# Kernel tuning notes

Hardware: AMD Instinct MI355X
Metric: run time of the kernel (lower is better)

## Reference

```python
import jax, jax.numpy as jnp
import numpy as np

B, N, M, H, NH = 8, 1024, 512, 1024, 4
DH = H // NH          # 256 main attention head size
CDH = (H // 4) // 4   # 64  cross attention qk head size
EPS = 1e-12


def _ln(x, g, b):
    mu = jnp.mean(x, axis=-1, keepdims=True)
    var = jnp.mean((x - mu) ** 2, axis=-1, keepdims=True)
    return (x - mu) / jnp.sqrt(var + EPS) * g + b


def _heads(x, nh):
    b, n, d = x.shape
    return x.reshape(b, n, nh, d // nh).transpose(0, 2, 1, 3)  # [b,nh,n,dh]


def setup_inputs() -> dict:
    key = jax.random.key(0)
    ks = iter(jax.random.split(key, 64))
    nk = lambda: next(ks)
    w = lambda *s: jax.random.normal(nk(), s, jnp.float32) * 0.02
    inp = {}
    inp["hidden_states"] = jax.random.normal(nk(), (B, N, H), jnp.float32)
    inp["attention_mask"] = jnp.ones((B, N), jnp.float32)
    inp["structure_mask"] = (jax.random.uniform(nk(), (B, 3, N, N)) < 0.2).astype(jnp.float32)
    inp["Sentence_em"] = w(1, B, N, H)
    inp["entity_id_em"] = w(1, B, N, H)
    inp["cross_struct_mask"] = (jax.random.uniform(nk(), (B, 1, N, M)) < 0.3).astype(jnp.float32)
    inp["encoder_hidden_states"] = jax.random.normal(nk(), (1, B, M, H), jnp.float32)
    inp["encoder_attention_mask"] = jnp.ones((B, M), jnp.float32)
    # ---- Struct_SelfAttention params ----
    inp["Wq"] = w(H, 3 * DH); inp["bq"] = jnp.zeros(3 * DH)
    inp["Wk"] = w(H, 3 * DH); inp["bk"] = jnp.zeros(3 * DH)
    inp["Wv"] = w(H, H);      inp["bv"] = jnp.zeros(H)
    inp["Wq1"] = w(H, DH);    inp["bq1"] = jnp.zeros(DH)
    inp["Wk1"] = w(H, DH);    inp["bk1"] = jnp.zeros(DH)
    inp["ln_g"] = jnp.ones(H); inp["ln_b"] = jnp.zeros(H)
    inp["gnn_W"] = w(H, H); inp["gnn_b"] = jnp.zeros(H)
    inp["gnn_ln_g"] = jnp.ones(H); inp["gnn_ln_b"] = jnp.zeros(H)
    # ---- Cross_Attention params ----
    inp["cWq"] = w(H, H // 4); inp["cbq"] = jnp.zeros(H // 4)
    inp["cWk"] = w(H, H // 4); inp["cbk"] = jnp.zeros(H // 4)
    inp["cWv"] = w(H, H);      inp["cbv"] = jnp.zeros(H)
    inp["cWo"] = w(H, H);      inp["cbo"] = jnp.zeros(H)
    inp["cWg"] = w(2 * H, H);  inp["cbg"] = jnp.full((H,), -1.0, jnp.float32)  # Gate bias init -1
    inp["c_ln_g"] = jnp.ones(H); inp["c_ln_b"] = jnp.zeros(H)
    # ---- Output block params ----
    inp["oW1"] = w(H, H); inp["ob1"] = jnp.zeros(H)
    inp["o_ln1_g"] = jnp.ones(H); inp["o_ln1_b"] = jnp.zeros(H)
    inp["oW2"] = w(H, 2 * H); inp["ob2"] = jnp.zeros(2 * H)
    inp["oW3"] = w(2 * H, H); inp["ob3"] = jnp.zeros(H)
    inp["o_ln3_g"] = jnp.ones(H); inp["o_ln3_b"] = jnp.zeros(H)
    inp["layer_idx"] = 0
    return inp


def reference(hidden_states, attention_mask, structure_mask, Sentence_em, entity_id_em,
              cross_struct_mask, encoder_hidden_states, encoder_attention_mask,
              Wq, bq, Wk, bk, Wv, bv, Wq1, bq1, Wk1, bk1, ln_g, ln_b,
              gnn_W, gnn_b, gnn_ln_g, gnn_ln_b,
              cWq, cbq, cWk, cbk, cWv, cbv, cWo, cbo, cWg, cbg, c_ln_g, c_ln_b,
              oW1, ob1, o_ln1_g, o_ln1_b, oW2, ob2, oW3, ob3, o_ln3_g, o_ln3_b,
              layer_idx):
    hs = hidden_states
    q = _heads(hs @ Wq + bq, 3)          # [B,3,N,DH]
    k = _heads(hs @ Wk + bk, 3)
    v = _heads(hs @ Wv + bv, 4)          # [B,4,N,DH]
    s1 = jnp.einsum('bhnd,bhmd->bhnm', q, k)          # unscaled scores, 3 heads
    am0 = (1.0 - attention_mask)[:, None, None, :] * -10000.0
    s3 = s1 + am0
    # valid off-diagonal pairs mask (broadcasts over the 3 heads)
    pair = attention_mask[:, None, :, None] * attention_mask[:, None, None, :]
    idxw = ((pair * (1.0 - jnp.eye(N, dtype=jnp.float32))) > 0.5).astype(jnp.float32)  # [B,1,N,N]
    # sigmoid focal loss (gamma=2, alpha=0.25, mean over selected elements)
    p = jax.nn.sigmoid(s3)
    t = structure_mask
    fl = 0.25 * t * (1.0 - p) ** 2 * (-jax.nn.log_sigmoid(s3)) \
       + 0.75 * (1.0 - t) * p ** 2 * (-jax.nn.log_sigmoid(-s3))
    loss = jnp.sum(fl * idxw) / (3.0 * jnp.sum(idxw))
    # structural attention path (3 heads)
    s1 = s1 / np.float32(np.sqrt(DH)) + (1.0 - structure_mask) * -10000.0
    probs1 = jax.nn.softmax(s1, axis=-1)
    # positional/structural single-head path
    h1 = _ln(hs + Sentence_em[layer_idx] + entity_id_em[layer_idx], ln_g, ln_b)
    q1 = _heads(h1 @ Wq1 + bq1, 1)
    k1 = _heads(h1 @ Wk1 + bk1, 1)
    s2 = jnp.einsum('bhnd,bhmd->bhnm', q1, k1) / np.float32(np.sqrt(DH)) + am0
    probs2 = jax.nn.softmax(s2, axis=-1)
    probs = jnp.concatenate([probs2, probs1], axis=1)  # [B,4,N,N]
    ctx = jnp.einsum('bhnm,bhmd->bhnd', probs, v).transpose(0, 2, 1, 3).reshape(B, N, H)
    gnn_out = _ln(ctx @ gnn_W + gnn_b, gnn_ln_g, gnn_ln_b)
    # ---- Cross attention ----
    enc = encoder_hidden_states[layer_idx]            # [B,M,H]
    cq = _heads(gnn_out @ cWq + cbq, 4)               # [B,4,N,CDH]
    ck = _heads(enc @ cWk + cbk, 4)                   # [B,4,M,CDH]
    cv = _heads(enc @ cWv + cbv, 4)                   # [B,4,M,DH]
    cs = jnp.einsum('bhnd,bhmd->bhnm', cq, ck) / np.float32(np.sqrt(CDH))
    cs = cs + (1.0 - cross_struct_mask) * -10000.0
    cp = jax.nn.softmax(cs, axis=-1)
    cctx = jnp.einsum('bhnm,bhmd->bhnd', cp, cv).transpose(0, 2, 1, 3).reshape(B, N, H)
    cctx = cctx @ cWo + cbo
    gate = jax.nn.sigmoid(jnp.concatenate([gnn_out, cctx], axis=-1) @ cWg + cbg)
    cross_out = _ln(gate * cctx + (1.0 - gate) * gnn_out, c_ln_g, c_ln_b)
    # ---- Output block (gated FFN) ----
    h = _ln(cross_out @ oW1 + ob1 + hidden_states, o_ln1_g, o_ln1_b)
    h3 = jax.nn.gelu(h @ oW2 + ob2, approximate=False) @ oW3 + ob3
    out = _ln(h3 + h, o_ln3_g, o_ln3_b)
    return out, loss
```

## Files before the change

### kernel.cpp

```cpp
#include <hip/hip_runtime.h>
#include <math.h>

#define DEV __device__ __forceinline__

typedef short short8 __attribute__((ext_vector_type(8)));
typedef float float4v __attribute__((ext_vector_type(4)));

DEV unsigned short f2bf(float f) {
    union { float f; unsigned u; } v; v.f = f;
    unsigned r = v.u + 0x7FFFu + ((v.u >> 16) & 1u);
    return (unsigned short)(r >> 16);
}

DEV float block_reduce(float v, int mode) {
    #pragma unroll
    for (int off = 32; off; off >>= 1) {
        float o = __shfl_xor(v, off);
        v = mode ? fmaxf(v, o) : (v + o);
    }
    __shared__ float sbuf[4];
    __syncthreads();
    if ((threadIdx.x & 63) == 0) sbuf[threadIdx.x >> 6] = v;
    __syncthreads();
    float r = sbuf[0];
    #pragma unroll
    for (int w = 1; w < 4; w++) r = mode ? fmaxf(r, sbuf[w]) : (r + sbuf[w]);
    return r;
}

template <bool BIAS, bool ACCUM, bool GELU>
__global__ __launch_bounds__(256) void gemm_bf16_kernel(
    const unsigned short* __restrict__ A, int lda,
    const unsigned short* __restrict__ Bt, int ldb,
    const float* __restrict__ bias,
    float* __restrict__ Cf, unsigned short* __restrict__ Cb,
    int N, int K)
{
    __shared__ unsigned short As[128 * 40];
    __shared__ unsigned short Bs[128 * 40];
    const int tid = threadIdx.x;
    const int w = tid >> 6, lane = tid & 63;
    const int l15 = lane & 15, quad = lane >> 4;
    const int m0 = blockIdx.y * 128, n0 = blockIdx.x * 128;
    const int wm = (w >> 1) * 64, wn = (w & 1) * 64;

    float4v acc[4][4];
    #pragma unroll
    for (int i = 0; i < 4; i++)
        #pragma unroll
        for (int j = 0; j < 4; j++) acc[i][j] = (float4v){0.f, 0.f, 0.f, 0.f};

    for (int k0 = 0; k0 < K; k0 += 32) {
        __syncthreads();
        #pragma unroll
        for (int i = 0; i < 2; i++) {
            const int c = tid + i * 256;
            const int row = c >> 2, kc = (c & 3) * 8;
            *(uint4*)(As + row * 40 + kc) =
                *(const uint4*)(A + (size_t)(m0 + row) * lda + k0 + kc);
            *(uint4*)(Bs + row * 40 + kc) =
                *(const uint4*)(Bt + (size_t)(n0 + row) * ldb + k0 + kc);
        }
        __syncthreads();
        short8 Af[4], Bf[4];
        #pragma unroll
        for (int mt = 0; mt < 4; mt++)
            Af[mt] = *(const short8*)(As + (wm + mt * 16 + l15) * 40 + quad * 8);
        #pragma unroll
        for (int nt = 0; nt < 4; nt++)
            Bf[nt] = *(const short8*)(Bs + (wn + nt * 16 + l15) * 40 + quad * 8);
        #pragma unroll
        for (int mt = 0; mt < 4; mt++)
            #pragma unroll
            for (int nt = 0; nt < 4; nt++)
                acc[mt][nt] = __builtin_amdgcn_mfma_f32_16x16x32_bf16(
                    Af[mt], Bf[nt], acc[mt][nt], 0, 0, 0);
    }

    #pragma unroll
    for (int nt = 0; nt < 4; nt++) {
        const int n = n0 + wn + nt * 16 + l15;
        const float bv = BIAS ? bias[n] : 0.f;
        #pragma unroll
        for (int mt = 0; mt < 4; mt++) {
            #pragma unroll
            for (int r = 0; r < 4; r++) {
                const int m = m0 + wm + mt * 16 + quad * 4 + r;
                const size_t off = (size_t)m * N + n;
                float v = acc[mt][nt][r] + bv;
                if (ACCUM) v += Cf[off];
                if (GELU) v = 0.5f * v * (1.f + erff(v * 0.70710678118654752f));
                if (Cf) Cf[off] = v;
                if (Cb) Cb[off] = f2bf(v);
            }
        }
    }
}

__global__ __launch_bounds__(256) void wtrans_kernel(
    const float* __restrict__ W, unsigned short* __restrict__ Wt, int K, int N)
{
    __shared__ float t[32][33];
    const int n0 = blockIdx.x * 32, k0 = blockIdx.y * 32;
    const int c = threadIdx.x & 31, r8 = threadIdx.x >> 5;
    #pragma unroll
    for (int i = 0; i < 4; i++) {
        const int r = r8 + i * 8;
        t[r][c] = W[(size_t)(k0 + r) * N + n0 + c];
    }
    __syncthreads();
    #pragma unroll
    for (int i = 0; i < 4; i++) {
        const int r = r8 + i * 8;
        Wt[(size_t)(n0 + r) * K + k0 + c] = f2bf(t[c][r]);
    }
}

__global__ __launch_bounds__(256) void trans_kernel(
    const unsigned short* __restrict__ v, unsigned short* __restrict__ Vt,
    int R, int C)
{
    __shared__ unsigned short t[32][33];
    const int b = blockIdx.z, r0 = blockIdx.x * 32, c0 = blockIdx.y * 32;
    const int c = threadIdx.x & 31, r8 = threadIdx.x >> 5;
    #pragma unroll
    for (int i = 0; i < 4; i++) {
        const int r = r8 + i * 8;
        t[r][c] = v[((size_t)b * R + r0 + r) * C + c0 + c];
    }
    __syncthreads();
    #pragma unroll
    for (int i = 0; i < 4; i++) {
        const int r = r8 + i * 8;
        Vt[((size_t)b * C + c0 + r) * R + r0 + c] = t[c][r];
    }
}

__global__ __launch_bounds__(256) void castbf_kernel(
    const float* __restrict__ x, unsigned short* __restrict__ y)
{
    const size_t i = ((size_t)blockIdx.x * 256 + threadIdx.x) * 4;
    float4 v = *(const float4*)(x + i);
    ushort4 o;
    o.x = f2bf(v.x); o.y = f2bf(v.y); o.z = f2bf(v.z); o.w = f2bf(v.w);
    *(ushort4*)(y + i) = o;
}

DEV void ln_finish(float4 xv, const float* __restrict__ g,
                   const float* __restrict__ bb, float* __restrict__ outf,
                   unsigned short* __restrict__ outb, size_t base)
{
    float s  = xv.x + xv.y + xv.z + xv.w;
    float s2 = xv.x * xv.x + xv.y * xv.y + xv.z * xv.z + xv.w * xv.w;
    #pragma unroll
    for (int off = 32; off; off >>= 1) {
        s += __shfl_xor(s, off);
        s2 += __shfl_xor(s2, off);
    }
    __shared__ float sa[4], sb[4];
    if ((threadIdx.x & 63) == 0) {
        sa[threadIdx.x >> 6] = s; sb[threadIdx.x >> 6] = s2;
    }
    __syncthreads();
    s  = sa[0] + sa[1] + sa[2] + sa[3];
    s2 = sb[0] + sb[1] + sb[2] + sb[3];
    const float mu  = s * (1.f / 1024.f);
    const float var = fmaxf(s2 * (1.f / 1024.f) - mu * mu, 0.f);
    const float inv = rsqrtf(var + 1e-12f);
    const int tid = threadIdx.x;
    float4 gv = ((const float4*)g)[tid];
    float4 bv = ((const float4*)bb)[tid];
    float4 o;
    o.x = (xv.x - mu) * inv * gv.x + bv.x;
    o.y = (xv.y - mu) * inv * gv.y + bv.y;
    o.z = (xv.z - mu) * inv * gv.z + bv.z;
    o.w = (xv.w - mu) * inv * gv.w + bv.w;
    if (outf) ((float4*)(outf + base))[tid] = o;
    if (outb) {
        ushort4 ob;
        ob.x = f2bf(o.x); ob.y = f2bf(o.y); ob.z = f2bf(o.z); ob.w = f2bf(o.w);
        ((ushort4*)(outb + base))[tid] = ob;
    }
}

__global__ __launch_bounds__(256) void ln_kernel(
    const float* __restrict__ x, const float* __restrict__ r1,
    const float* __restrict__ r2, const float* __restrict__ g,
    const float* __restrict__ bb, float* __restrict__ outf,
    unsigned short* __restrict__ outb)
{
    const size_t base = (size_t)blockIdx.x * 1024;
    const int tid = threadIdx.x;
    float4 xv = ((const float4*)(x + base))[tid];
    if (r1) {
        float4 a = ((const float4*)(r1 + base))[tid];
        xv.x += a.x; xv.y += a.y; xv.z += a.z; xv.w += a.w;
    }
    if (r2) {
        float4 a = ((const float4*)(r2 + base))[tid];
        xv.x += a.x; xv.y += a.y; xv.z += a.z; xv.w += a.w;
    }
    ln_finish(xv, g, bb, outf, outb, base);
}

__global__ __launch_bounds__(256) void gate_ln_kernel(
    const float* __restrict__ gpre, const float* __restrict__ co,
    const float* __restrict__ gn, const float* __restrict__ g,
    const float* __restrict__ bb, float* __restrict__ outf,
    unsigned short* __restrict__ outb)
{
    const size_t base = (size_t)blockIdx.x * 1024;
    const int tid = threadIdx.x;
    float4 gp = ((const float4*)(gpre + base))[tid];
    float4 cv = ((const float4*)(co + base))[tid];
    float4 gv = ((const float4*)(gn + base))[tid];
    float4 xv; float s;
    s = 1.f / (1.f + __expf(-gp.x)); xv.x = s * cv.x + (1.f - s) * gv.x;
    s = 1.f / (1.f + __expf(-gp.y)); xv.y = s * cv.y + (1.f - s) * gv.y;
    s = 1.f / (1.f + __expf(-gp.z)); xv.z = s * cv.z + (1.f - s) * gv.z;
    s = 1.f / (1.f + __expf(-gp.w)); xv.w = s * cv.w + (1.f - s) * gv.w;
    ln_finish(xv, g, bb, outf, outb, base);
}

__global__ __launch_bounds__(256) void attn_mfma_kernel(
    const unsigned short* __restrict__ qh,
    const unsigned short* __restrict__ kh,
    const unsigned short* __restrict__ q1,
    const unsigned short* __restrict__ k1,
    const unsigned short* __restrict__ Vt,
    const float* __restrict__ am,
    const float* __restrict__ smask,
    unsigned short* __restrict__ ctx,
    float* __restrict__ nump, float* __restrict__ denp)
{
    const int nb = blockIdx.x;
    const int h  = blockIdx.y;
    const int b  = blockIdx.z;
    const int tid = threadIdx.x;
    const int w = tid >> 6, lane = tid & 63;
    const int l15 = lane & 15, quad = lane >> 4;
    const int n0 = nb * 64;

    __shared__ unsigned short Ks[32 * 264];
    __shared__ unsigned short Vs[256 * 40];
    __shared__ unsigned short Ps[4][16 * 40];

    const unsigned short* qsrc; const unsigned short* ksrc; int kpitch, koff;
    if (h == 0) { qsrc = q1; ksrc = k1; kpitch = 256; koff = 0; }
    else        { qsrc = qh; ksrc = kh; kpitch = 768; koff = (h - 1) * 256; }

    short8 Qf[8];
    {
        const unsigned short* qrow =
            qsrc + (size_t)(b * 1024 + n0 + w * 16 + l15) * kpitch + koff;
        #pragma unroll
        for (int kk = 0; kk < 8; kk++)
            Qf[kk] = *(const short8*)(qrow + kk * 32 + quad * 8);
    }

    float4v O[16];
    #pragma unroll
    for (int i = 0; i < 16; i++) O[i] = (float4v){0.f, 0.f, 0.f, 0.f};
    float lsum[4] = {0.f, 0.f, 0.f, 0.f};
    float flsum = 0.f, dencnt = 0.f;
    const int nrow_base = n0 + w * 16 + quad * 4;
    float amn[4];
    #pragma unroll
    for (int r = 0; r < 4; r++) amn[r] = am[b * 1024 + nrow_base + r];
    const float* smbase = (h > 0)
        ? smask + ((size_t)b * 3 + (h - 1)) * 1024 * 1024 : nullptr;

    for (int m0 = 0; m0 < 1024; m0 += 32) {
        __syncthreads();
        for (int c = tid; c < 1024; c += 256) {
            const int row = c >> 5, kc = (c & 31) * 8;
            *(uint4*)(Ks + row * 264 + kc) =
                *(const uint4*)(ksrc + (size_t)(b * 1024 + m0 + row) * kpitch + koff + kc);
        }
        for (int c = tid; c < 1024; c += 256) {
            const int d = c >> 2, mc = (c & 3) * 8;
            *(uint4*)(Vs + d * 40 + mc) =
                *(const uint4*)(Vt + (size_t)(b * 1024 + h * 256 + d) * 1024 + m0 + mc);
        }
        __syncthreads();

        float4v S[2];
        #pragma unroll
        for (int st = 0; st < 2; st++) {
            float4v a = (float4v){0.f, 0.f, 0.f, 0.f};
            #pragma unroll
            for (int kk = 0; kk < 8; kk++) {
                short8 Kf = *(const short8*)(Ks + (st * 16 + l15) * 264 + kk * 32 + quad * 8);
                a = __builtin_amdgcn_mfma_f32_16x16x32_bf16(Qf[kk], Kf, a, 0, 0, 0);
            }
            S[st] = a;
        }

        float e[2][4];
        #pragma unroll
        for (int st = 0; st < 2; st++) {
            const int mcol = m0 + st * 16 + l15;
            const float amm = am[b * 1024 + mcol];
            const float am0 = (1.f - amm) * (-10000.f);
            #pragma unroll
            for (int r = 0; r < 4; r++) {
                const float sraw = S[st][r];
                float scv;
                if (h > 0) {
                    const int nrow = nrow_base + r;
                    const float t  = smbase[(size_t)nrow * 1024 + mcol];
                    const float s3 = sraw + am0;
                    const float idxw =
                        ((amn[r] * amm * ((mcol == nrow) ? 0.f : 1.f)) > 0.5f) ? 1.f : 0.f;
                    const float E = __expf(-fabsf(s3));
                    const float L = __logf(1.f + E);
                    const float R = 1.f / (1.f + E);
                    const float p = (s3 >= 0.f) ? R : E * R;
                    const float sp = fmaxf(s3, 0.f) + L;
                    const float omp = 1.f - p;
                    flsum += idxw * (0.25f * t * omp * omp * (sp - s3)
                                   + 0.75f * (1.f - t) * p * p * sp);
                    dencnt += idxw;
                    scv = sraw * 0.0625f + (1.f - t) * (-10000.f);
                } else {
                    scv = sraw * 0.0625f + am0;
                }
                const float ev = __expf(fminf(scv, 30.f));
                e[st][r] = ev;
                lsum[r] += ev;
            }
        }

        #pragma unroll
        for (int st = 0; st < 2; st++)
            #pragma unroll
            for (int r = 0; r < 4; r++)
                Ps[w][(quad * 4 + r) * 40 + st * 16 + l15] = f2bf(e[st][r]);
        const short8 Pf = *(const short8*)(&Ps[w][l15 * 40 + quad * 8]);
        #pragma unroll
        for (int dt = 0; dt < 16; dt++) {
            short8 Vf = *(const short8*)(Vs + (dt * 16 + l15) * 40 + quad * 8);
            O[dt] = __builtin_amdgcn_mfma_f32_16x16x32_bf16(Pf, Vf, O[dt], 0, 0, 0);
        }
    }

    float rinv[4];
    #pragma unroll
    for (int r = 0; r < 4; r++) {
        float s = lsum[r];
        #pragma unroll
        for (int off = 8; off; off >>= 1) s += __shfl_xor(s, off);
        rinv[r] = 1.f / s;
    }
    #pragma unroll
    for (int dt = 0; dt < 16; dt++)
        #pragma unroll
        for (int r = 0; r < 4; r++)
            ctx[(size_t)(b * 1024 + nrow_base + r) * 1024 + h * 256 + dt * 16 + l15]
                = f2bf(O[dt][r] * rinv[r]);

    if (h > 0) {
        const float fb = block_reduce(flsum, 0);
        if (tid == 0) nump[(b * 3 + (h - 1)) * 16 + nb] = fb;
        if (h == 1) {
            const float db = block_reduce(dencnt, 0);
            if (tid == 0) denp[b * 16 + nb] = db;
        }
    }
}

__global__ __launch_bounds__(256) void cross_mfma_kernel(
    const unsigned short* __restrict__ cq,
    const unsigned short* __restrict__ ck,
    const unsigned short* __restrict__ cvt,
    const float* __restrict__ csm,
    unsigned short* __restrict__ cctx)
{
    const int nb = blockIdx.x;
    const int h  = blockIdx.y;
    const int b  = blockIdx.z;
    const int tid = threadIdx.x;
    const int w = tid >> 6, lane = tid & 63;
    const int l15 = lane & 15, quad = lane >> 4;
    const int n0 = nb * 64;

    __shared__ unsigned short Ks[32 * 72];
    __shared__ unsigned short Vs[256 * 40];
    __shared__ unsigned short Ps[4][16 * 40];

    short8 Qf[2];
    {
        const unsigned short* qrow =
            cq + (size_t)(b * 1024 + n0 + w * 16 + l15) * 256 + h * 64;
        #pragma unroll
        for (int kk = 0; kk < 2; kk++)
            Qf[kk] = *(const short8*)(qrow + kk * 32 + quad * 8);
    }

    float4v O[16];
    #pragma unroll
    for (int i = 0; i < 16; i++) O[i] = (float4v){0.f, 0.f, 0.f, 0.f};
    float lsum[4] = {0.f, 0.f, 0.f, 0.f};
    const int nrow_base = n0 + w * 16 + quad * 4;

    for (int m0 = 0; m0 < 512; m0 += 32) {
        __syncthreads();
        if (tid < 256) {
            const int row = tid >> 3, kc = (tid & 7) * 8;
            *(uint4*)(Ks + row * 72 + kc) =
                *(const uint4*)(ck + (size_t)(b * 512 + m0 + row) * 256 + h * 64 + kc);
        }
        for (int c = tid; c < 1024; c += 256) {
            const int d = c >> 2, mc = (c & 3) * 8;
            *(uint4*)(Vs + d * 40 + mc) =
                *(const uint4*)(cvt + (size_t)(b * 1024 + h * 256 + d) * 512 + m0 + mc);
        }
        __syncthreads();

        float e[2][4];
        #pragma unroll
        for (int st = 0; st < 2; st++) {
            float4v a = (float4v){0.f, 0.f, 0.f, 0.f};
            #pragma unroll
            for (int kk = 0; kk < 2; kk++) {
                short8 Kf = *(const short8*)(Ks + (st * 16 + l15) * 72 + kk * 32 + quad * 8);
                a = __builtin_amdgcn_mfma_f32_16x16x32_bf16(Qf[kk], Kf, a, 0, 0, 0);
            }
            const int mcol = m0 + st * 16 + l15;
            #pragma unroll
            for (int r = 0; r < 4; r++) {
                const float msk = csm[(size_t)(b * 1024 + nrow_base + r) * 512 + mcol];
                const float scv = a[r] * 0.125f + (1.f - msk) * (-10000.f);
                const float ev = __expf(fminf(scv, 30.f));
                e[st][r] = ev;
                lsum[r] += ev;
            }
        }

        #pragma unroll
        for (int st = 0; st < 2; st++)
            #pragma unroll
            for (int r = 0; r < 4; r++)
                Ps[w][(quad * 4 + r) * 40 + st * 16 + l15] = f2bf(e[st][r]);
        const short8 Pf = *(const short8*)(&Ps[w][l15 * 40 + quad * 8]);
        #pragma unroll
        for (int dt = 0; dt < 16; dt++) {
            short8 Vf = *(const short8*)(Vs + (dt * 16 + l15) * 40 + quad * 8);
            O[dt] = __builtin_amdgcn_mfma_f32_16x16x32_bf16(Pf, Vf, O[dt], 0, 0, 0);
        }
    }

    float rinv[4];
    #pragma unroll
    for (int r = 0; r < 4; r++) {
        float s = lsum[r];
        #pragma unroll
        for (int off = 8; off; off >>= 1) s += __shfl_xor(s, off);
        rinv[r] = 1.f / s;
    }
    #pragma unroll
    for (int dt = 0; dt < 16; dt++)
        #pragma unroll
        for (int r = 0; r < 4; r++)
            cctx[(size_t)(b * 1024 + nrow_base + r) * 1024 + h * 256 + dt * 16 + l15]
                = f2bf(O[dt][r] * rinv[r]);
}

__global__ __launch_bounds__(256) void loss_reduce_kernel(
    const float* __restrict__ nump, const float* __restrict__ denp,
    float* __restrict__ out)
{
    __shared__ double sn[256], sd[256];
    const int tid = threadIdx.x;
    double ns = 0.0, ds = 0.0;
    for (int i = tid; i < 384; i += 256) ns += (double)nump[i];
    for (int i = tid; i < 128; i += 256) ds += (double)denp[i];
    sn[tid] = ns; sd[tid] = ds;
    __syncthreads();
    for (int off = 128; off; off >>= 1) {
        if (tid < off) { sn[tid] += sn[tid + off]; sd[tid] += sd[tid + off]; }
        __syncthreads();
    }
    if (tid == 0) out[0] = (float)(sn[0] / (3.0 * sd[0]));
}

extern "C" void kernel_launch(void* const* d_in, const int* in_sizes, int n_in,
                              void* d_out, int out_size, void* d_ws, size_t ws_size,
                              hipStream_t stream)
{
    (void)in_sizes; (void)n_in; (void)out_size; (void)ws_size;
    const float* hs   = (const float*)d_in[0];
    const float* am   = (const float*)d_in[1];
    const float* smask= (const float*)d_in[2];
    const float* sent = (const float*)d_in[3];
    const float* ent  = (const float*)d_in[4];
    const float* csm  = (const float*)d_in[5];
    const float* enc  = (const float*)d_in[6];
    const float* Wq  = (const float*)d_in[8];  const float* bq  = (const float*)d_in[9];
    const float* Wk  = (const float*)d_in[10]; const float* bk  = (const float*)d_in[11];
    const float* Wv  = (const float*)d_in[12]; const float* bv  = (const float*)d_in[13];
    const float* Wq1 = (const float*)d_in[14]; const float* bq1 = (const float*)d_in[15];
    const float* Wk1 = (const float*)d_in[16]; const float* bk1 = (const float*)d_in[17];
    const float* ln_g= (const float*)d_in[18]; const float* ln_b= (const float*)d_in[19];
    const float* gW  = (const float*)d_in[20]; const float* gb  = (const float*)d_in[21];
    const float* gng = (const float*)d_in[22]; const float* gnb = (const float*)d_in[23];
    const float* cWq = (const float*)d_in[24]; const float* cbq = (const float*)d_in[25];
    const float* cWk = (const float*)d_in[26]; const float* cbk = (const float*)d_in[27];
    const float* cWv = (const float*)d_in[28]; const float* cbv = (const float*)d_in[29];
    const float* cWo = (const float*)d_in[30]; const float* cbo = (const float*)d_in[31];
    const float* cWg = (const float*)d_in[32]; const float* cbg = (const float*)d_in[33];
    const float* clg = (const float*)d_in[34]; const float* clb = (const float*)d_in[35];
    const float* oW1 = (const float*)d_in[36]; const float* ob1 = (const float*)d_in[37];
    const float* l1g = (const float*)d_in[38]; const float* l1b = (const float*)d_in[39];
    const float* oW2 = (const float*)d_in[40]; const float* ob2 = (const float*)d_in[41];
    const float* oW3 = (const float*)d_in[42]; const float* ob3 = (const float*)d_in[43];
    const float* l3g = (const float*)d_in[44]; const float* l3b = (const float*)d_in[45];
    float* out = (float*)d_out;

    typedef unsigned short ush;
    char* wsb = (char*)d_ws;
    ush* WT   = (ush*)wsb;
    ush* wqT  = WT;             ush* wkT  = WT + 786432;   ush* wvT  = WT + 1572864;
    ush* wq1T = WT + 2621440;   ush* wk1T = WT + 2883584;  ush* gWT_ = WT + 3145728;
    ush* cWqT = WT + 4194304;   ush* cWkT = WT + 4456448;  ush* cWvT = WT + 4718592;
    ush* cWoT = WT + 5767168;   ush* cWgT = WT + 6815744;  ush* oW1T = WT + 8912896;
    ush* oW2T = WT + 9961472;   ush* oW3T = WT + 12058624;
    ush*  hs_bf   = (ush*)(wsb + 28311552);
    ush*  enc_bf  = (ush*)(wsb + 45088768);
    ush*  q_bf    = (ush*)(wsb + 53477376);
    ush*  k_bf    = (ush*)(wsb + 66060288);
    ush*  v_bf    = (ush*)(wsb + 78643200);
    ush*  Vt      = (ush*)(wsb + 95420416);
    ush*  h1_bf   = (ush*)(wsb + 112197632);
    ush*  q1_bf   = (ush*)(wsb + 128974848);
    ush*  k1_bf   = (ush*)(wsb + 133169152);
    ush*  ctx_bf  = (ush*)(wsb + 137363456);
    float* nump   = (float*)(wsb + 154140672);
    float* denp   = (float*)(wsb + 154142208);
    float* gnn_f  = (float*)(wsb + 154144768);
    float* gnnout_f = (float*)(wsb + 187699200);
    ush*  gnnout_b  = (ush*)(wsb + 221253632);
    ush*  cq_b      = (ush*)(wsb + 53477376);
    ush*  ck_b      = (ush*)(wsb + 66060288);
    ush*  cv_b      = (ush*)(wsb + 78643200);
    ush*  cctx_b    = (ush*)(wsb + 95420416);
    ush*  cvt       = (ush*)(wsb + 238030848);
    float* cctxo_f  = (float*)(wsb + 154144768);
    ush*  cctxo_b   = (ush*)(wsb + 28311552);
    float* gatepre_f= (float*)(wsb + 112197632);
    ush*  crossout_b= (ush*)(wsb + 221253632);
    float* t_f      = (float*)(wsb + 154144768);
    float* h_f      = (float*)(wsb + 187699200);
    ush*  h_b       = (ush*)(wsb + 28311552);
    ush*  h2g_b     = (ush*)(wsb + 45088768);
    float* h3_f     = (float*)(wsb + 154144768);

    dim3 blk(256);
    castbf_kernel<<<8192, blk, 0, stream>>>(hs, hs_bf);
    castbf_kernel<<<4096, blk, 0, stream>>>(enc, enc_bf);
    wtrans_kernel<<<dim3(768/32, 1024/32), blk, 0, stream>>>(Wq, wqT, 1024, 768);
    wtrans_kernel<<<dim3(768/32, 1024/32), blk, 0, stream>>>(Wk, wkT, 1024, 768);
    wtrans_kernel<<<dim3(32, 32), blk, 0, stream>>>(Wv, wvT, 1024, 1024);
    wtrans_kernel<<<dim3(8, 32), blk, 0, stream>>>(Wq1, wq1T, 1024, 256);
    wtrans_kernel<<<dim3(8, 32), blk, 0, stream>>>(Wk1, wk1T, 1024, 256);
    wtrans_kernel<<<dim3(32, 32), blk, 0, stream>>>(gW, gWT_, 1024, 1024);
    wtrans_kernel<<<dim3(8, 32), blk, 0, stream>>>(cWq, cWqT, 1024, 256);
    wtrans_kernel<<<dim3(8, 32), blk, 0, stream>>>(cWk, cWkT, 1024, 256);
    wtrans_kernel<<<dim3(32, 32), blk, 0, stream>>>(cWv, cWvT, 1024, 1024);
    wtrans_kernel<<<dim3(32, 32), blk, 0, stream>>>(cWo, cWoT, 1024, 1024);
    wtrans_kernel<<<dim3(32, 64), blk, 0, stream>>>(cWg, cWgT, 2048, 1024);
    wtrans_kernel<<<dim3(32, 32), blk, 0, stream>>>(oW1, oW1T, 1024, 1024);
    wtrans_kernel<<<dim3(64, 32), blk, 0, stream>>>(oW2, oW2T, 1024, 2048);
    wtrans_kernel<<<dim3(32, 64), blk, 0, stream>>>(oW3, oW3T, 2048, 1024);
    gemm_bf16_kernel<true,false,false><<<dim3(6, 64), blk, 0, stream>>>(
        hs_bf, 1024, wqT, 1024, bq, nullptr, q_bf, 768, 1024);
    gemm_bf16_kernel<true,false,false><<<dim3(6, 64), blk, 0, stream>>>(
        hs_bf, 1024, wkT, 1024, bk, nullptr, k_bf, 768, 1024);
    gemm_bf16_kernel<true,false,false><<<dim3(8, 64), blk, 0, stream>>>(
        hs_bf, 1024, wvT, 1024, bv, nullptr, v_bf, 1024, 1024);
    ln_kernel<<<8192, blk, 0, stream>>>(hs, sent, ent, ln_g, ln_b, nullptr, h1_bf);
    gemm_bf16_kernel<true,false,false><<<dim3(2, 64), blk, 0, stream>>>(
        h1_bf, 1024, wq1T, 1024, bq1, nullptr, q1_bf, 256, 1024);
    gemm_bf16_kernel<true,false,false><<<dim3(2, 64), blk, 0, stream>>>(
        h1_bf, 1024, wk1T, 1024, bk1, nullptr, k1_bf, 256, 1024);
    trans_kernel<<<dim3(32, 32, 8), blk, 0, stream>>>(v_bf, Vt, 1024, 1024);
    attn_mfma_kernel<<<dim3(16, 4, 8), blk, 0, stream>>>(
        q_bf, k_bf, q1_bf, k1_bf, Vt, am, smask, ctx_bf, nump, denp);
    loss_reduce_kernel<<<1, blk, 0, stream>>>(nump, denp, out + 8388608);
    gemm_bf16_kernel<true,false,false><<<dim3(8, 64), blk, 0, stream>>>(
        ctx_bf, 1024, gWT_, 1024, gb, gnn_f, nullptr, 1024, 1024);
    ln_kernel<<<8192, blk, 0, stream>>>(gnn_f, nullptr, nullptr, gng, gnb,
                                        gnnout_f, gnnout_b);
    gemm_bf16_kernel<true,false,false><<<dim3(2, 64), blk, 0, stream>>>(
        gnnout_b, 1024, cWqT, 1024, cbq, nullptr, cq_b, 256, 1024);
    gemm_bf16_kernel<true,false,false><<<dim3(2, 32), blk, 0, stream>>>(
        enc_bf, 1024, cWkT, 1024, cbk, nullptr, ck_b, 256, 1024);
    gemm_bf16_kernel<true,false,false><<<dim3(8, 32), blk, 0, stream>>>(
        enc_bf, 1024, cWvT, 1024, cbv, nullptr, cv_b, 1024, 1024);
    trans_kernel<<<dim3(16, 32, 8), blk, 0, stream>>>(cv_b, cvt, 512, 1024);
    cross_mfma_kernel<<<dim3(16, 4, 8), blk, 0, stream>>>(
        cq_b, ck_b, cvt, csm, cctx_b);
    gemm_bf16_kernel<true,false,false><<<dim3(8, 64), blk, 0, stream>>>(
        cctx_b, 1024, cWoT, 1024, cbo, cctxo_f, cctxo_b, 1024, 1024);
    gemm_bf16_kernel<true,false,false><<<dim3(8, 64), blk, 0, stream>>>(
        gnnout_b, 1024, cWgT, 2048, cbg, gatepre_f, nullptr, 1024, 1024);
    gemm_bf16_kernel<false,true,false><<<dim3(8, 64), blk, 0, stream>>>(
        cctxo_b, 1024, cWgT + 1024, 2048, nullptr, gatepre_f, nullptr, 1024, 1024);
    gate_ln_kernel<<<8192, blk, 0, stream>>>(gatepre_f, cctxo_f, gnnout_f,
                                             clg, clb, nullptr, crossout_b);
    gemm_bf16_kernel<true,false,false><<<dim3(8, 64), blk, 0, stream>>>(
        crossout_b, 1024, oW1T, 1024, ob1, t_f, nullptr, 1024, 1024);
    ln_kernel<<<8192, blk, 0, stream>>>(t_f, hs, nullptr, l1g, l1b, h_f, h_b);
    gemm_bf16_kernel<true,false,true><<<dim3(16, 64), blk, 0, stream>>>(
        h_b, 1024, oW2T, 1024, ob2, nullptr, h2g_b, 2048, 1024);
    gemm_bf16_kernel<true,false,false><<<dim3(8, 64), blk, 0, stream>>>(
        h2g_b, 2048, oW3T, 2048, ob3, h3_f, nullptr, 1024, 2048);
    ln_kernel<<<8192, blk, 0, stream>>>(h3_f, h_f, nullptr, l3g, l3b, out, nullptr);
}
```

Baseline: 1.310 ms.

## Fuse QKV projections, use async LDS loads in GEMM, stream K/V from global in attention

Result: slower. 1.470 ms (+12.2%).

```diff
diff --git a/kernel.cpp b/kernel.cpp
--- a/kernel.cpp
+++ b/kernel.cpp
@@ -12,63 +12,65 @@
     return (unsigned short)(r >> 16);
 }
 
-DEV float block_reduce(float v, int mode) {
-    #pragma unroll
-    for (int off = 32; off; off >>= 1) {
-        float o = __shfl_xor(v, off);
-        v = mode ? fmaxf(v, o) : (v + o);
-    }
-    __shared__ float sbuf[4];
+DEV void async16(const unsigned short* g, unsigned short* l) {
+    __builtin_amdgcn_global_load_lds(
+        (const __attribute__((address_space(1))) unsigned int*)g,
+        (__attribute__((address_space(3))) unsigned int*)l, 16, 0, 0);
+}
+
+DEV float block_reduce128(float v) {
+    #pragma unroll
+    for (int off = 32; off; off >>= 1) v += __shfl_xor(v, off);
+    __shared__ float sbuf[2];
     __syncthreads();
     if ((threadIdx.x & 63) == 0) sbuf[threadIdx.x >> 6] = v;
     __syncthreads();
-    float r = sbuf[0];
-    #pragma unroll
-    for (int w = 1; w < 4; w++) r = mode ? fmaxf(r, sbuf[w]) : (r + sbuf[w]);
-    return r;
+    return sbuf[0] + sbuf[1];
 }
 
 template <bool BIAS, bool ACCUM, bool GELU>
 __global__ __launch_bounds__(256) void gemm_bf16_kernel(
     const unsigned short* __restrict__ A, int lda,
     const unsigned short* __restrict__ Bt, int ldb,
-    const float* __restrict__ bias,
+    const float* __restrict__ bias, const float* __restrict__ bias2,
+    const float* __restrict__ bias3, int ns1, int ns2,
     float* __restrict__ Cf, unsigned short* __restrict__ Cb,
     int N, int K)
 {
-    __shared__ unsigned short As[128 * 40];
-    __shared__ unsigned short Bs[128 * 40];
+    __shared__ unsigned short As[128 * 32];
+    __shared__ unsigned short Bs[128 * 32];
     const int tid = threadIdx.x;
     const int w = tid >> 6, lane = tid & 63;
     const int l15 = lane & 15, quad = lane >> 4;
     const int m0 = blockIdx.y * 128, n0 = blockIdx.x * 128;
     const int wm = (w >> 1) * 64, wn = (w & 1) * 64;
+    const int lr = lane >> 2, lc = (lane & 3) * 8;
 
     float4v acc[4][4];
     #pragma unroll
     for (int i = 0; i < 4; i++)
         #pragma unroll
         for (int j = 0; j < 4; j++) acc[i][j] = (float4v){0.f, 0.f, 0.f, 0.f};
+
+    const unsigned short* Ab = A  + (size_t)(m0 + w * 16 + lr) * lda + lc;
+    const unsigned short* Bb = Bt + (size_t)(n0 + w * 16 + lr) * ldb + lc;
+    unsigned short* AsW = As + (w * 16) * 32;
+    unsigned short* BsW = Bs + (w * 16) * 32;
 
     for (int k0 = 0; k0 < K; k0 += 32) {
         __syncthreads();
-        #pragma unroll
-        for (int i = 0; i < 2; i++) {
-            const int c = tid + i * 256;
-            const int row = c >> 2, kc = (c & 3) * 8;
-            *(uint4*)(As + row * 40 + kc) =
-                *(const uint4*)(A + (size_t)(m0 + row) * lda + k0 + kc);
-            *(uint4*)(Bs + row * 40 + kc) =
-                *(const uint4*)(Bt + (size_t)(n0 + row) * ldb + k0 + kc);
-        }
+        async16(Ab + k0, AsW);
+        async16(Ab + (size_t)64 * lda + k0, AsW + 64 * 32);
+        async16(Bb + k0, BsW);
+        async16(Bb + (size_t)64 * ldb + k0, BsW + 64 * 32);
         __syncthreads();
         short8 Af[4], Bf[4];
         #pragma unroll
         for (int mt = 0; mt < 4; mt++)
-            Af[mt] = *(const short8*)(As + (wm + mt * 16 + l15) * 40 + quad * 8);
+            Af[mt] = *(const short8*)(As + (wm + mt * 16 + l15) * 32 + quad * 8);
         #pragma unroll
         for (int nt = 0; nt < 4; nt++)
-            Bf[nt] = *(const short8*)(Bs + (wn + nt * 16 + l15) * 40 + quad * 8);
+            Bf[nt] = *(const short8*)(Bs + (wn + nt * 16 + l15) * 32 + quad * 8);
         #pragma unroll
         for (int mt = 0; mt < 4; mt++)
             #pragma unroll
@@ -80,7 +82,9 @@
     #pragma unroll
     for (int nt = 0; nt < 4; nt++) {
         const int n = n0 + wn + nt * 16 + l15;
-        const float bv = BIAS ? bias[n] : 0.f;
+        float bv = 0.f;
+        if (BIAS) bv = (n < ns1) ? bias[n] : (n < ns2) ? bias2[n - ns1]
+                                                       : bias3[n - ns2];
         #pragma unroll
         for (int mt = 0; mt < 4; mt++) {
             #pragma unroll
@@ -118,7 +122,7 @@
 
 __global__ __launch_bounds__(256) void trans_kernel(
     const unsigned short* __restrict__ v, unsigned short* __restrict__ Vt,
-    int R, int C)
+    int R, int C, int vpitch, int voff)
 {
     __shared__ unsigned short t[32][33];
     const int b = blockIdx.z, r0 = blockIdx.x * 32, c0 = blockIdx.y * 32;
@@ -126,7 +130,7 @@
     #pragma unroll
     for (int i = 0; i < 4; i++) {
         const int r = r8 + i * 8;
-        t[r][c] = v[((size_t)b * R + r0 + r) * C + c0 + c];
+        t[r][c] = v[((size_t)b * R + r0 + r) * vpitch + voff + c0 + c];
     }
     __syncthreads();
     #pragma unroll
@@ -222,41 +226,41 @@
     ln_finish(xv, g, bb, outf, outb, base);
 }
 
-__global__ __launch_bounds__(256) void attn_mfma_kernel(
-    const unsigned short* __restrict__ qh,
-    const unsigned short* __restrict__ kh,
-    const unsigned short* __restrict__ q1,
-    const unsigned short* __restrict__ k1,
+__global__ __launch_bounds__(128, 3) void attn_mfma_kernel(
+    const unsigned short* __restrict__ qkv,
+    const unsigned short* __restrict__ q1k1,
     const unsigned short* __restrict__ Vt,
     const float* __restrict__ am,
     const float* __restrict__ smask,
     unsigned short* __restrict__ ctx,
     float* __restrict__ nump, float* __restrict__ denp)
 {
-    const int nb = blockIdx.x;
-    const int h  = blockIdx.y;
-    const int b  = blockIdx.z;
+    const int bid0 = blockIdx.x + 32 * (blockIdx.y + 4 * blockIdx.z);
+    const int bid = (bid0 & 7) * 128 + (bid0 >> 3);
+    const int nb = bid & 31;
+    const int h  = (bid >> 5) & 3;
+    const int b  = bid >> 7;
     const int tid = threadIdx.x;
     const int w = tid >> 6, lane = tid & 63;
     const int l15 = lane & 15, quad = lane >> 4;
-    const int n0 = nb * 64;
-
-    __shared__ unsigned short Ks[32 * 264];
-    __shared__ unsigned short Vs[256 * 40];
-    __shared__ unsigned short Ps[4][16 * 40];
-
-    const unsigned short* qsrc; const unsigned short* ksrc; int kpitch, koff;
-    if (h == 0) { qsrc = q1; ksrc = k1; kpitch = 256; koff = 0; }
-    else        { qsrc = qh; ksrc = kh; kpitch = 768; koff = (h - 1) * 256; }
+    const int n0 = nb * 32;
+
+    __shared__ unsigned short Ps[2][16 * 40];
+
+    const unsigned short* qsrc; const unsigned short* ksrc; int pitch;
+    if (h == 0) { qsrc = q1k1;               ksrc = q1k1 + 256;             pitch = 512; }
+    else        { qsrc = qkv + (h - 1) * 256; ksrc = qkv + 768 + (h - 1) * 256; pitch = 2560; }
 
     short8 Qf[8];
     {
         const unsigned short* qrow =
-            qsrc + (size_t)(b * 1024 + n0 + w * 16 + l15) * kpitch + koff;
+            qsrc + (size_t)(b * 1024 + n0 + w * 16 + l15) * pitch;
         #pragma unroll
         for (int kk = 0; kk < 8; kk++)
             Qf[kk] = *(const short8*)(qrow + kk * 32 + quad * 8);
     }
+    const unsigned short* kbase = ksrc + ((size_t)(b * 1024) + l15) * pitch + quad * 8;
+    const unsigned short* vbase = Vt + (size_t)(b * 1024 + h * 256 + l15) * 1024 + quad * 8;
 
     float4v O[16];
     #pragma unroll
@@ -264,33 +268,22 @@
     float lsum[4] = {0.f, 0.f, 0.f, 0.f};
     float flsum = 0.f, dencnt = 0.f;
     const int nrow_base = n0 + w * 16 + quad * 4;
+    const float* amrow = am + b * 1024;
     float amn[4];
     #pragma unroll
-    for (int r = 0; r < 4; r++) amn[r] = am[b * 1024 + nrow_base + r];
+    for (int r = 0; r < 4; r++) amn[r] = amrow[nrow_base + r];
     const float* smbase = (h > 0)
         ? smask + ((size_t)b * 3 + (h - 1)) * 1024 * 1024 : nullptr;
 
     for (int m0 = 0; m0 < 1024; m0 += 32) {
-        __syncthreads();
-        for (int c = tid; c < 1024; c += 256) {
-            const int row = c >> 5, kc = (c & 31) * 8;
-            *(uint4*)(Ks + row * 264 + kc) =
-                *(const uint4*)(ksrc + (size_t)(b * 1024 + m0 + row) * kpitch + koff + kc);
-        }
-        for (int c = tid; c < 1024; c += 256) {
-            const int d = c >> 2, mc = (c & 3) * 8;
-            *(uint4*)(Vs + d * 40 + mc) =
-                *(const uint4*)(Vt + (size_t)(b * 1024 + h * 256 + d) * 1024 + m0 + mc);
-        }
-        __syncthreads();
-
         float4v S[2];
         #pragma unroll
         for (int st = 0; st < 2; st++) {
             float4v a = (float4v){0.f, 0.f, 0.f, 0.f};
+            const unsigned short* kr = kbase + (size_t)(m0 + st * 16) * pitch;
             #pragma unroll
             for (int kk = 0; kk < 8; kk++) {
-                short8 Kf = *(const short8*)(Ks + (st * 16 + l15) * 264 + kk * 32 + quad * 8);
+                short8 Kf = *(const short8*)(kr + kk * 32);
                 a = __builtin_amdgcn_mfma_f32_16x16x32_bf16(Qf[kk], Kf, a, 0, 0, 0);
             }
             S[st] = a;
@@ -300,7 +293,7 @@
         #pragma unroll
         for (int st = 0; st < 2; st++) {
             const int mcol = m0 + st * 16 + l15;
-            const float amm = am[b * 1024 + mcol];
+            const float amm = amrow[mcol];
             const float am0 = (1.f - amm) * (-10000.f);
             #pragma unroll
             for (int r = 0; r < 4; r++) {
@@ -339,7 +332,7 @@
         const short8 Pf = *(const short8*)(&Ps[w][l15 * 40 + quad * 8]);
         #pragma unroll
         for (int dt = 0; dt < 16; dt++) {
-            short8 Vf = *(const short8*)(Vs + (dt * 16 + l15) * 40 + quad * 8);
+            short8 Vf = *(const short8*)(vbase + (size_t)dt * 16384 + m0);
             O[dt] = __builtin_amdgcn_mfma_f32_16x16x32_bf16(Pf, Vf, O[dt], 0, 0, 0);
         }
     }
@@ -360,33 +353,33 @@
                 = f2bf(O[dt][r] * rinv[r]);
 
     if (h > 0) {
-        const float fb = block_reduce(flsum, 0);
-        if (tid == 0) nump[(b * 3 + (h - 1)) * 16 + nb] = fb;
+        const float fb = block_reduce128(flsum);
+        if (tid == 0) nump[((b * 3) + (h - 1)) * 32 + nb] = fb;
         if (h == 1) {
-            const float db = block_reduce(dencnt, 0);
-            if (tid == 0) denp[b * 16 + nb] = db;
-        }
-    }
-}
-
-__global__ __launch_bounds__(256) void cross_mfma_kernel(
+            const float db = block_reduce128(dencnt);
+            if (tid == 0) denp[b * 32 + nb] = db;
+        }
+    }
+}
+
+__global__ __launch_bounds__(128, 4) void cross_mfma_kernel(
     const unsigned short* __restrict__ cq,
-    const unsigned short* __restrict__ ck,
+    const unsigned short* __restrict__ ckv,
     const unsigned short* __restrict__ cvt,
     const float* __restrict__ csm,
     unsigned short* __restrict__ cctx)
 {
-    const int nb = blockIdx.x;
-    const int h  = blockIdx.y;
-    const int b  = blockIdx.z;
+    const int bid0 = blockIdx.x + 32 * (blockIdx.y + 4 * blockIdx.z);
+    const int bid = (bid0 & 7) * 128 + (bid0 >> 3);
+    const int nb = bid & 31;
+    const int h  = (bid >> 5) & 3;
+    const int b  = bid >> 7;
     const int tid = threadIdx.x;
     const int w = tid >> 6, lane = tid & 63;
     const int l15 = lane & 15, quad = lane >> 4;
-    const int n0 = nb * 64;
-
-    __shared__ unsigned short Ks[32 * 72];
-    __shared__ unsigned short Vs[256 * 40];
-    __shared__ unsigned short Ps[4][16 * 40];
+    const int n0 = nb * 32;
+
+    __shared__ unsigned short Ps[2][16 * 40];
 
     short8 Qf[2];
     {
@@ -396,6 +389,8 @@
         for (int kk = 0; kk < 2; kk++)
             Qf[kk] = *(const short8*)(qrow + kk * 32 + quad * 8);
     }
+    const unsigned short* kbase = ckv + ((size_t)(b * 512) + l15) * 1280 + h * 64 + quad * 8;
+    const unsigned short* vbase = cvt + (size_t)(b * 1024 + h * 256 + l15) * 512 + quad * 8;
 
     float4v O[16];
     #pragma unroll
@@ -404,26 +399,14 @@
     const int nrow_base = n0 + w * 16 + quad * 4;
 
     for (int m0 = 0; m0 < 512; m0 += 32) {
-        __syncthreads();
-        if (tid < 256) {
-            const int row = tid >> 3, kc = (tid & 7) * 8;
-            *(uint4*)(Ks + row * 72 + kc) =
-                *(const uint4*)(ck + (size_t)(b * 512 + m0 + row) * 256 + h * 64 + kc);
-        }
-        for (int c = tid; c < 1024; c += 256) {
-            const int d = c >> 2, mc = (c & 3) * 8;
-            *(uint4*)(Vs + d * 40 + mc) =
-                *(const uint4*)(cvt + (size_t)(b * 1024 + h * 256 + d) * 512 + m0 + mc);
-        }
-        __syncthreads();
-
         float e[2][4];
         #pragma unroll
         for (int st = 0; st < 2; st++) {
             float4v a = (float4v){0.f, 0.f, 0.f, 0.f};
+            const unsigned short* kr = kbase + (size_t)(m0 + st * 16) * 1280;
             #pragma unroll
             for (int kk = 0; kk < 2; kk++) {
-                short8 Kf = *(const short8*)(Ks + (st * 16 + l15) * 72 + kk * 32 + quad * 8);
+                short8 Kf = *(const short8*)(kr + kk * 32);
                 a = __builtin_amdgcn_mfma_f32_16x16x32_bf16(Qf[kk], Kf, a, 0, 0, 0);
             }
             const int mcol = m0 + st * 16 + l15;
@@ -445,7 +428,7 @@
         const short8 Pf = *(const short8*)(&Ps[w][l15 * 40 + quad * 8]);
         #pragma unroll
         for (int dt = 0; dt < 16; dt++) {
-            short8 Vf = *(const short8*)(Vs + (dt * 16 + l15) * 40 + quad * 8);
+            short8 Vf = *(const short8*)(vbase + (size_t)dt * 8192 + m0);
             O[dt] = __builtin_amdgcn_mfma_f32_16x16x32_bf16(Pf, Vf, O[dt], 0, 0, 0);
         }
     }
@@ -473,8 +456,8 @@
     __shared__ double sn[256], sd[256];
     const int tid = threadIdx.x;
     double ns = 0.0, ds = 0.0;
-    for (int i = tid; i < 384; i += 256) ns += (double)nump[i];
-    for (int i = tid; i < 128; i += 256) ds += (double)denp[i];
+    for (int i = tid; i < 768; i += 256) ns += (double)nump[i];
+    for (int i = tid; i < 256; i += 256) ds += (double)denp[i];
     sn[tid] = ns; sd[tid] = ds;
     __syncthreads();
     for (int off = 128; off; off >>= 1) {
@@ -525,24 +508,21 @@
     ush* cWqT = WT + 4194304;   ush* cWkT = WT + 4456448;  ush* cWvT = WT + 4718592;
     ush* cWoT = WT + 5767168;   ush* cWgT = WT + 6815744;  ush* oW1T = WT + 8912896;
     ush* oW2T = WT + 9961472;   ush* oW3T = WT + 12058624;
+    (void)wkT; (void)wvT; (void)wk1T; (void)cWvT;
     ush*  hs_bf   = (ush*)(wsb + 28311552);
     ush*  enc_bf  = (ush*)(wsb + 45088768);
-    ush*  q_bf    = (ush*)(wsb + 53477376);
-    ush*  k_bf    = (ush*)(wsb + 66060288);
-    ush*  v_bf    = (ush*)(wsb + 78643200);
+    ush*  qkv_bf  = (ush*)(wsb + 53477376);
     ush*  Vt      = (ush*)(wsb + 95420416);
     ush*  h1_bf   = (ush*)(wsb + 112197632);
-    ush*  q1_bf   = (ush*)(wsb + 128974848);
-    ush*  k1_bf   = (ush*)(wsb + 133169152);
+    ush*  q1k1_bf = (ush*)(wsb + 128974848);
     ush*  ctx_bf  = (ush*)(wsb + 137363456);
     float* nump   = (float*)(wsb + 154140672);
-    float* denp   = (float*)(wsb + 154142208);
+    float* denp   = (float*)(wsb + 154143744);
     float* gnn_f  = (float*)(wsb + 154144768);
     float* gnnout_f = (float*)(wsb + 187699200);
     ush*  gnnout_b  = (ush*)(wsb + 221253632);
     ush*  cq_b      = (ush*)(wsb + 53477376);
-    ush*  ck_b      = (ush*)(wsb + 66060288);
-    ush*  cv_b      = (ush*)(wsb + 78643200);
+    ush*  ckv_b     = (ush*)(wsb + 66060288);
     ush*  cctx_b    = (ush*)(wsb + 95420416);
     ush*  cvt       = (ush*)(wsb + 238030848);
     float* cctxo_f  = (float*)(wsb + 154144768);
@@ -555,7 +535,8 @@
     ush*  h2g_b     = (ush*)(wsb + 45088768);
     float* h3_f     = (float*)(wsb + 154144768);
 
-    dim3 blk(256);
+    const int BIG = 1 << 30;
+    dim3 blk(256), blk128(128);
     castbf_kernel<<<8192, blk, 0, stream>>>(hs, hs_bf);
     castbf_kernel<<<4096, blk, 0, stream>>>(enc, enc_bf);
     wtrans_kernel<<<dim3(768/32, 1024/32), blk, 0, stream>>>(Wq, wqT, 1024, 768);
@@ -572,48 +553,40 @@
     wtrans_kernel<<<dim3(32, 32), blk, 0, stream>>>(oW1, oW1T, 1024, 1024);
     wtrans_kernel<<<dim3(64, 32), blk, 0, stream>>>(oW2, oW2T, 1024, 2048);
     wtrans_kernel<<<dim3(32, 64), blk, 0, stream>>>(oW3, oW3T, 2048, 1024);
-    gemm_bf16_kernel<true,false,false><<<dim3(6, 64), blk, 0, stream>>>(
-        hs_bf, 1024, wqT, 1024, bq, nullptr, q_bf, 768, 1024);
-    gemm_bf16_kernel<true,false,false><<<dim3(6, 64), blk, 0, stream>>>(
-        hs_bf, 1024, wkT, 1024, bk, nullptr, k_bf, 768, 1024);
-    gemm_bf16_kernel<true,false,false><<<dim3(8, 64), blk, 0, stream>>>(
-        hs_bf, 1024, wvT, 1024, bv, nullptr, v_bf, 1024, 1024);
+    gemm_bf16_kernel<true,false,false><<<dim3(20, 64), blk, 0, stream>>>(
+        hs_bf, 1024, wqT, 1024, bq, bk, bv, 768, 1536, nullptr, qkv_bf, 2560, 1024);
     ln_kernel<<<8192, blk, 0, stream>>>(hs, sent, ent, ln_g, ln_b, nullptr, h1_bf);
-    gemm_bf16_kernel<true,false,false><<<dim3(2, 64), blk, 0, stream>>>(
-        h1_bf, 1024, wq1T, 1024, bq1, nullptr, q1_bf, 256, 1024);
-    gemm_bf16_kernel<true,false,false><<<dim3(2, 64), blk, 0, stream>>>(
-        h1_bf, 1024, wk1T, 1024, bk1, nullptr, k1_bf, 256, 1024);
-    trans_kernel<<<dim3(32, 32, 8), blk, 0, stream>>>(v_bf, Vt, 1024, 1024);
-    attn_mfma_kernel<<<dim3(16, 4, 8), blk, 0, stream>>>(
-        q_bf, k_bf, q1_bf, k1_bf, Vt, am, smask, ctx_bf, nump, denp);
+    gemm_bf16_kernel<true,false,false><<<dim3(4, 64), blk, 0, stream>>>(
+        h1_bf, 1024, wq1T, 1024, bq1, bk1, nullptr, 256, BIG, nullptr, q1k1_bf, 512, 1024);
+    trans_kernel<<<dim3(32, 32, 8), blk, 0, stream>>>(qkv_bf, Vt, 1024, 1024, 2560, 1536);
+    attn_mfma_kernel<<<dim3(32, 4, 8), blk128, 0, stream>>>(
+        qkv_bf, q1k1_bf, Vt, am, smask, ctx_bf, nump, denp);
     loss_reduce_kernel<<<1, blk, 0, stream>>>(nump, denp, out + 8388608);
     gemm_bf16_kernel<true,false,false><<<dim3(8, 64), blk, 0, stream>>>(
-        ctx_bf, 1024, gWT_, 1024, gb, gnn_f, nullptr, 1024, 1024);
+        ctx_bf, 1024, gWT_, 1024, gb, nullptr, nullptr, BIG, BIG, gnn_f, nullptr, 1024, 1024);
     ln_kernel<<<8192, blk, 0, stream>>>(gnn_f, nullptr, nullptr, gng, gnb,
                                         gnnout_f, gnnout_b);
     gemm_bf16_kernel<true,false,false><<<dim3(2, 64), blk, 0, stream>>>(
-        gnnout_b, 1024, cWqT, 1024, cbq, nullptr, cq_b, 256, 1024);
-    gemm_bf16_kernel<true,false,false><<<dim3(2, 32), blk, 0, stream>>>(
-        enc_bf, 1024, cWkT, 1024, cbk, nullptr, ck_b, 256, 1024);
-    gemm_bf16_kernel<true,false,false><<<dim3(8, 32), blk, 0, stream>>>(
-        enc_bf, 1024, cWvT, 1024, cbv, nullptr, cv_b, 1024, 1024);
-    trans_kernel<<<dim3(16, 32, 8), blk, 0, stream>>>(cv_b, cvt, 512, 1024);
-    cross_mfma_kernel<<<dim3(16, 4, 8), blk, 0, stream>>>(
-        cq_b, ck_b, cvt, csm, cctx_b);
+        gnnout_b, 1024, cWqT, 1024, cbq, nullptr, nullptr, BIG, BIG, nullptr, cq_b, 256, 1024);
+    gemm_bf16_kernel<true,false,false><<<dim3(10, 32), blk, 0, stream>>>(
+        enc_bf, 1024, cWkT, 1024, cbk, cbv, nullptr, 256, BIG, nullptr, ckv_b, 1280, 1024);
+    trans_kernel<<<dim3(16, 32, 8), blk, 0, stream>>>(ckv_b, cvt, 512, 1024, 1280, 256);
+    cross_mfma_kernel<<<dim3(32, 4, 8), blk128, 0, stream>>>(
+        cq_b, ckv_b, cvt, csm, cctx_b);
     gemm_bf16_kernel<true,false,false><<<dim3(8, 64), blk, 0, stream>>>(
-        cctx_b, 1024, cWoT, 1024, cbo, cctxo_f, cctxo_b, 1024, 1024);
+        cctx_b, 1024, cWoT, 1024, cbo, nullptr, nullptr, BIG, BIG, cctxo_f, cctxo_b, 1024, 1024);
     gemm_bf16_kernel<true,false,false><<<dim3(8, 64), blk, 0, stream>>>(
-        gnnout_b, 1024, cWgT, 2048, cbg, gatepre_f, nullptr, 1024, 1024);
+        gnnout_b, 1024, cWgT, 2048, cbg, nullptr, nullptr, BIG, BIG, gatepre_f, nullptr, 1024, 1024);
     gemm_bf16_kernel<false,true,false><<<dim3(8, 64), blk, 0, stream>>>(
-        cctxo_b, 1024, cWgT + 1024, 2048, nullptr, gatepre_f, nullptr, 1024, 1024);
+        cctxo_b, 1024, cWgT + 1024, 2048, nullptr, nullptr, nullptr, BIG, BIG, gatepre_f, nullptr, 1024, 1024);
     gate_ln_kernel<<<8192, blk, 0, stream>>>(gatepre_f, cctxo_f, gnnout_f,
                                              clg, clb, nullptr, crossout_b);
     gemm_bf16_kernel<true,false,false><<<dim3(8, 64), blk, 0, stream>>>(
-        crossout_b, 1024, oW1T, 1024, ob1, t_f, nullptr, 1024, 1024);
+        crossout_b, 1024, oW1T, 1024, ob1, nullptr, nullptr, BIG, BIG, t_f, nullptr, 1024, 1024);
     ln_kernel<<<8192, blk, 0, stream>>>(t_f, hs, nullptr, l1g, l1b, h_f, h_b);
     gemm_bf16_kernel<true,false,true><<<dim3(16, 64), blk, 0, stream>>>(
-        h_b, 1024, oW2T, 1024, ob2, nullptr, h2g_b, 2048, 1024);
+        h_b, 1024, oW2T, 1024, ob2, nullptr, nullptr, BIG, BIG, nullptr, h2g_b, 2048, 1024);
     gemm_bf16_kernel<true,false,false><<<dim3(8, 64), blk, 0, stream>>>(
-        h2g_b, 2048, oW3T, 2048, ob3, h3_f, nullptr, 1024, 2048);
+        h2g_b, 2048, oW3T, 2048, ob3, nullptr, nullptr, BIG, BIG, h3_f, nullptr, 1024, 2048);
     ln_kernel<<<8192, blk, 0, stream>>>(h3_f, h_f, nullptr, l3g, l3b, out, nullptr);
 }
```
